# Performance work log

Measured on AMD Instinct MI355X. Metric: run time of the kernel, lower is better.

Reference implementation:

```python
import jax, jax.numpy as jnp
import numpy as np

INDIM, HID, OUTDIM, T = 28, 128, 10, 28

def setup_inputs() -> dict:
    key = jax.random.key(0)
    ks = jax.random.split(key, 7)
    B = 65536
    bound1 = 1.0 / np.sqrt(INDIM)
    bound2 = 1.0 / np.sqrt(2 * HID)
    bound3 = 1.0 / np.sqrt(HID)
    return {
        "x": jax.random.normal(ks[0], (B, 784), dtype=jnp.float32),
        "W1": jax.random.uniform(ks[1], (INDIM, HID), jnp.float32, -bound1, bound1),
        "b1": jax.random.uniform(ks[2], (HID,), jnp.float32, -bound1, bound1),
        "W2": jax.random.uniform(ks[3], (2 * HID, HID), jnp.float32, -bound2, bound2),
        "b2": jax.random.uniform(ks[4], (HID,), jnp.float32, -bound2, bound2),
        "W3": jax.random.uniform(ks[5], (HID, OUTDIM), jnp.float32, -bound3, bound3),
        "b3": jax.random.uniform(ks[6], (OUTDIM,), jnp.float32, -bound3, bound3),
    }

def reference(x, W1, b1, W2, b2, W3, b3):
    B = x.shape[0]
    # (B, 784) -> (T, B, 28): scan over the 28 rows of each image
    rows = jnp.transpose(x.reshape(B, T, INDIM), (1, 0, 2))
    # W2 split: first HID rows multiply linear1 output, last HID rows multiply hidden state
    W2a, W2b = W2[:HID], W2[HID:]

    def step(h, row):
        t = row @ W1 + b1                      # (B, HID)
        h_new = jax.nn.relu(t @ W2a + h @ W2b + b2)  # concat(t, h) @ W2 == t@W2a + h@W2b
        return h_new, None

    h0 = jnp.zeros((B, HID), dtype=x.dtype)
    h_final, _ = jax.lax.scan(step, h0, rows)
    return h_final @ W3 + b3
```

## Files before the change

kernel.cpp:

```cpp
#include <hip/hip_runtime.h>

#define BTOT 65536
#define TST  28
#define PACK_DW 180
#define WXL_OFF (64 * PACK_DW)

typedef __attribute__((ext_vector_type(8))) short bf16x8;
typedef __attribute__((ext_vector_type(4))) float f32x4;

__device__ __forceinline__ unsigned int f2bf(float f) {
    unsigned u = __float_as_uint(f);
    u += 0x7fff + ((u >> 16) & 1);
    return u >> 16;
}
__device__ __forceinline__ unsigned int pk2bf(float a, float b) {
    return f2bf(a) | (f2bf(b) << 16);
}
__device__ __forceinline__ bf16x8 cvt8(f32x4 a, f32x4 b) {
    union { unsigned int u[4]; bf16x8 v; } r;
    asm("v_cvt_pk_bf16_f32 %0, %1, %2" : "=v"(r.u[0]) : "v"(a[0]), "v"(a[1]));
    asm("v_cvt_pk_bf16_f32 %0, %1, %2" : "=v"(r.u[1]) : "v"(a[2]), "v"(a[3]));
    asm("v_cvt_pk_bf16_f32 %0, %1, %2" : "=v"(r.u[2]) : "v"(b[0]), "v"(b[1]));
    asm("v_cvt_pk_bf16_f32 %0, %1, %2" : "=v"(r.u[3]) : "v"(b[2]), "v"(b[3]));
    return r.v;
}


__global__ void pack1(const float* __restrict__ W1, const float* __restrict__ b1,
                      const float* __restrict__ W2, const float* __restrict__ b2,
                      const float* __restrict__ W3, const float* __restrict__ b3,
                      unsigned int* __restrict__ ws) {
    float* WxL = (float*)(ws + WXL_OFF);
    const int bid = blockIdx.x, tid = threadIdx.x;
    if (bid < 29) {
        const int k = bid, n = tid;
        float s = 0.f;
        if (k < 28) {
            for (int m = 0; m < 128; ++m) s += W1[k * 128 + m] * W2[m * 128 + n];
        } else {
            s = b2[n];
            for (int m = 0; m < 128; ++m) s += b1[m] * W2[m * 128 + n];
        }
        WxL[k * 128 + n] = s;
        if (k == 28) { WxL[29*128+n] = 0.f; WxL[30*128+n] = 0.f; WxL[31*128+n] = 0.f; }
    } else if (bid == 29) {
        if (tid < 64) {
            const int lr = tid & 15, kh = tid >> 4;
            unsigned int* P = ws + tid * PACK_DW;
            for (int kk = 0; kk < 4; ++kk)
                for (int t8 = 0; t8 < 8; ++t8)
                    for (int jd = 0; jd < 4; ++jd) {
                        const int s = kk * 32 + (jd >> 1) * 16 + kh * 4 + (jd & 1) * 2;
                        const int n = t8 * 16 + lr;
                        P[(kk * 8 + t8) * 4 + jd] =
                            pk2bf(W2[(128 + s) * 128 + n], W2[(129 + s) * 128 + n]);
                    }
        }
    } else {
        if (tid < 64) {
            const int lr = tid & 15, kh = tid >> 4;
            unsigned int* P = ws + tid * PACK_DW;
            for (int kk = 0; kk < 4; ++kk)
                for (int jd = 0; jd < 4; ++jd) {
                    const int s = kk * 32 + (jd >> 1) * 16 + kh * 4 + (jd & 1) * 2;
                    float lo = (lr < 10) ? W3[s * 10 + lr] : 0.f;
                    float hi = (lr < 10) ? W3[(s + 1) * 10 + lr] : 0.f;
                    P[160 + kk * 4 + jd] = pk2bf(lo, hi);
                }
            for (int j = 0; j < 4; ++j) {
                const int o = kh * 4 + j;
                P[176 + j] = __float_as_uint((o < 10) ? b3[o] : 0.f);
            }
        }
    }
}

__global__ void pack2(unsigned int* __restrict__ ws) {
    const int tid = threadIdx.x;
    if (tid < 64) {
        const float* WxL = (const float*)(ws + WXL_OFF);
        const int lr = tid & 15, kh = tid >> 4;
        unsigned int* P = ws + tid * PACK_DW;
        for (int t8 = 0; t8 < 8; ++t8)
            for (int jd = 0; jd < 4; ++jd) {
                const int k = kh * 8 + jd * 2, n = t8 * 16 + lr;
                P[128 + t8 * 4 + jd] = pk2bf(WxL[k * 128 + n], WxL[(k + 1) * 128 + n]);
            }
    }
}

__global__ __launch_bounds__(64, 2) void rnn_kernel(
    const float* __restrict__ x, const unsigned int* __restrict__ wsPack,
    float* __restrict__ out)
{
    const int lane = threadIdx.x;
    const int lr = lane & 15, kh = lane >> 4;
    const int r0 = blockIdx.x * 16;

    const unsigned int* P = wsPack + lane * PACK_DW;
    bf16x8 w2b[4][8], wx[8];
    #pragma unroll
    for (int kk = 0; kk < 4; ++kk)
        #pragma unroll
        for (int t8 = 0; t8 < 8; ++t8)
            w2b[kk][t8] = *(const bf16x8*)(P + (kk * 8 + t8) * 4);
    #pragma unroll
    for (int t8 = 0; t8 < 8; ++t8) wx[t8] = *(const bf16x8*)(P + 128 + t8 * 4);

    const f32x4 onec = {1.f, 0.f, 0.f, 0.f};
    const float* xr = x + (size_t)(r0 + lr) * 784 + 8 * kh;
    f32x4 xa = *(const f32x4*)xr;
    f32x4 xc = (kh < 3) ? *(const f32x4*)(xr + 4) : onec;
    bf16x8 xb = cvt8(xa, xc);
    const f32x4 z4 = {0.f, 0.f, 0.f, 0.f};

    f32x4 acc[8];
    union HF { unsigned int u[4]; bf16x8 v; } hb[4];
    f32x4 na, nc;

#define CVT(T8) do {                                                        \
        f32x4 v = acc[T8];                                                  \
        v[0] = fmaxf(v[0], 0.f); v[1] = fmaxf(v[1], 0.f);                   \
        v[2] = fmaxf(v[2], 0.f); v[3] = fmaxf(v[3], 0.f);                   \
        unsigned lo, hi;                                                    \
        asm("v_cvt_pk_bf16_f32 %0, %1, %2" : "=v"(lo) : "v"(v[0]), "v"(v[1])); \
        asm("v_cvt_pk_bf16_f32 %0, %1, %2" : "=v"(hi) : "v"(v[2]), "v"(v[3])); \
        hb[(T8) >> 1].u[((T8) & 1) * 2]     = lo;                           \
        hb[(T8) >> 1].u[((T8) & 1) * 2 + 1] = hi;                           \
    } while (0)
#define CVTALL  CVT(0); CVT(1); CVT(2); CVT(3); CVT(4); CVT(5); CVT(6); CVT(7)

    {
        const float* xp = xr + 28;
        na = *(const f32x4*)xp;
        nc = (kh < 3) ? *(const f32x4*)(xp + 4) : onec;
        __builtin_amdgcn_s_setprio(1);
        #pragma unroll
        for (int t8 = 0; t8 < 8; ++t8)
            acc[t8] = __builtin_amdgcn_mfma_f32_16x16x32_bf16(wx[t8], xb, z4, 0, 0, 0);
        __builtin_amdgcn_s_setprio(0);
        xb = cvt8(na, nc);
        CVTALL;
    }

    #pragma unroll 2
    for (int t = 1; t < TST; ++t) {
        const bool pf = (t + 1 < TST);
        if (pf) {
            const float* xp = xr + (t + 1) * 28;
            na = *(const f32x4*)xp;
            nc = (kh < 3) ? *(const f32x4*)(xp + 4) : onec;
        }
        __builtin_amdgcn_s_setprio(1);
        #pragma unroll
        for (int t8 = 0; t8 < 8; ++t8)
            acc[t8] = __builtin_amdgcn_mfma_f32_16x16x32_bf16(wx[t8], xb, z4, 0, 0, 0);
        #pragma unroll
        for (int kk = 0; kk < 4; ++kk)
            #pragma unroll
            for (int t8 = 0; t8 < 8; ++t8)
                acc[t8] = __builtin_amdgcn_mfma_f32_16x16x32_bf16(w2b[kk][t8], hb[kk].v, acc[t8], 0, 0, 0);
        __builtin_amdgcn_s_setprio(0);
        if (pf) xb = cvt8(na, nc);
        CVTALL;
    }

    bf16x8 w3f[4];
    #pragma unroll
    for (int kk = 0; kk < 4; ++kk) w3f[kk] = *(const bf16x8*)(P + 160 + kk * 4);
    const float* bp = (const float*)(P + 176);
    f32x4 accO = {bp[0], bp[1], bp[2], bp[3]};
    #pragma unroll
    for (int kk = 0; kk < 4; ++kk)
        accO = __builtin_amdgcn_mfma_f32_16x16x32_bf16(w3f[kk], hb[kk].v, accO, 0, 0, 0);
    float* op = out + (size_t)(r0 + lr) * 10 + kh * 4;
    #pragma unroll
    for (int j = 0; j < 4; ++j)
        if (kh * 4 + j < 10) op[j] = accO[j];

#undef CVT
#undef CVTALL
}

extern "C" void kernel_launch(void* const* d_in, const int* in_sizes, int n_in,
                              void* d_out, int out_size, void* d_ws, size_t ws_size,
                              hipStream_t stream) {
    const float* x  = (const float*)d_in[0];
    const float* W1 = (const float*)d_in[1];
    const float* b1 = (const float*)d_in[2];
    const float* W2 = (const float*)d_in[3];
    const float* b2 = (const float*)d_in[4];
    const float* W3 = (const float*)d_in[5];
    const float* b3 = (const float*)d_in[6];
    unsigned int* ws = (unsigned int*)d_ws;

    pack1<<<31, 128, 0, stream>>>(W1, b1, W2, b2, W3, b3, ws);
    pack2<<<1, 64, 0, stream>>>(ws);
    rnn_kernel<<<BTOT / 16, 64, 0, stream>>>(x, ws, (float*)d_out);
}
```

Measured before the change: 71.75 us.

## Interleave input-projection MFMAs for next step with relu/bf16 conversion of current step

Moves the x-projection MFMAs (wx times xb) for step t+1 out of the critical recurrent chain and issues them right after each pair of hidden-state conversions, so they overlap with the VALU relu/convert work. The loop is now fully unrolled. Each recurrent step then starts directly with the dependent W2b MFMAs. This aims to shorten the serial per-step latency, at the cost of larger code size and possibly more register pressure from full unrolling.

After: 76.27 us. 6.3% more time.

```diff
diff --git a/kernel.cpp b/kernel.cpp
--- a/kernel.cpp
+++ b/kernel.cpp
@@ -89,6 +89,8 @@
     }
 }
 
+#define MFMA(a, b, c) __builtin_amdgcn_mfma_f32_16x16x32_bf16(a, b, c, 0, 0, 0)
+
 __global__ __launch_bounds__(64, 2) void rnn_kernel(
     const float* __restrict__ x, const unsigned int* __restrict__ wsPack,
     float* __restrict__ out)
@@ -128,22 +130,27 @@
         hb[(T8) >> 1].u[((T8) & 1) * 2]     = lo;                           \
         hb[(T8) >> 1].u[((T8) & 1) * 2 + 1] = hi;                           \
     } while (0)
-#define CVTALL  CVT(0); CVT(1); CVT(2); CVT(3); CVT(4); CVT(5); CVT(6); CVT(7)
+#define CVT_REFILL(PAIR) do {                                               \
+        CVT(2 * (PAIR)); CVT(2 * (PAIR) + 1);                               \
+        acc[2 * (PAIR)]     = MFMA(wx[2 * (PAIR)],     xb, z4);             \
+        acc[2 * (PAIR) + 1] = MFMA(wx[2 * (PAIR) + 1], xb, z4);             \
+    } while (0)
 
     {
         const float* xp = xr + 28;
         na = *(const f32x4*)xp;
         nc = (kh < 3) ? *(const f32x4*)(xp + 4) : onec;
-        __builtin_amdgcn_s_setprio(1);
-        #pragma unroll
-        for (int t8 = 0; t8 < 8; ++t8)
-            acc[t8] = __builtin_amdgcn_mfma_f32_16x16x32_bf16(wx[t8], xb, z4, 0, 0, 0);
-        __builtin_amdgcn_s_setprio(0);
+        #pragma unroll
+        for (int t8 = 0; t8 < 8; ++t8)
+            acc[t8] = MFMA(wx[t8], xb, z4);
         xb = cvt8(na, nc);
-        CVTALL;
-    }
-
-    #pragma unroll 2
+        CVT(0); CVT(1); CVT(2); CVT(3); CVT(4); CVT(5); CVT(6); CVT(7);
+        #pragma unroll
+        for (int t8 = 0; t8 < 8; ++t8)
+            acc[t8] = MFMA(wx[t8], xb, z4);
+    }
+
+    #pragma unroll
     for (int t = 1; t < TST; ++t) {
         const bool pf = (t + 1 < TST);
         if (pf) {
@@ -153,16 +160,17 @@
         }
         __builtin_amdgcn_s_setprio(1);
         #pragma unroll
-        for (int t8 = 0; t8 < 8; ++t8)
-            acc[t8] = __builtin_amdgcn_mfma_f32_16x16x32_bf16(wx[t8], xb, z4, 0, 0, 0);
-        #pragma unroll
         for (int kk = 0; kk < 4; ++kk)
             #pragma unroll
             for (int t8 = 0; t8 < 8; ++t8)
-                acc[t8] = __builtin_amdgcn_mfma_f32_16x16x32_bf16(w2b[kk][t8], hb[kk].v, acc[t8], 0, 0, 0);
+                acc[t8] = MFMA(w2b[kk][t8], hb[kk].v, acc[t8]);
         __builtin_amdgcn_s_setprio(0);
-        if (pf) xb = cvt8(na, nc);
-        CVTALL;
+        if (pf) {
+            xb = cvt8(na, nc);
+            CVT_REFILL(0); CVT_REFILL(1); CVT_REFILL(2); CVT_REFILL(3);
+        } else {
+            CVT(0); CVT(1); CVT(2); CVT(3); CVT(4); CVT(5); CVT(6); CVT(7);
+        }
     }
 
     bf16x8 w3f[4];
@@ -172,14 +180,14 @@
     f32x4 accO = {bp[0], bp[1], bp[2], bp[3]};
     #pragma unroll
     for (int kk = 0; kk < 4; ++kk)
-        accO = __builtin_amdgcn_mfma_f32_16x16x32_bf16(w3f[kk], hb[kk].v, accO, 0, 0, 0);
+        accO = MFMA(w3f[kk], hb[kk].v, accO);
     float* op = out + (size_t)(r0 + lr) * 10 + kh * 4;
     #pragma unroll
     for (int j = 0; j < 4; ++j)
         if (kh * 4 + j < 10) op[j] = accO[j];
 
 #undef CVT
-#undef CVTALL
+#undef CVT_REFILL
 }
 
 extern "C" void kernel_launch(void* const* d_in, const int* in_sizes, int n_in,
```

## Switch recurrence to 32x32x16 MFMA tiles with 32 rows per wave

Applied to the files above, without the earlier changes.

Replaces the 16x16x32 bf16 MFMA formulation with 32x32x16 tiles, so each wave processes 32 batch rows instead of 16 and the grid halves. All weight packs are re-laid out for the new operand fragment layout, and the input-projection weights are staged in LDS rather than kept in registers, to make room for the larger accumulators. The aim is higher MFMA throughput per instruction and better reuse of the register-resident W2 fragments across more rows. The trade-offs are higher register pressure from the 16-wide accumulators, extra LDS reads every step, and fewer waves available to hide latency.

Result: slower. 85.64 us (+19.4%).

```diff
diff --git a/kernel.cpp b/kernel.cpp
--- a/kernel.cpp
+++ b/kernel.cpp
@@ -2,11 +2,13 @@
 
 #define BTOT 65536
 #define TST  28
-#define PACK_DW 180
+#define PACK_DW 208
 #define WXL_OFF (64 * PACK_DW)
 
-typedef __attribute__((ext_vector_type(8))) short bf16x8;
-typedef __attribute__((ext_vector_type(4))) float f32x4;
+typedef __attribute__((ext_vector_type(8)))  short bf16x8;
+typedef __attribute__((ext_vector_type(4)))  float f32x4;
+typedef __attribute__((ext_vector_type(16))) float f32x16;
+typedef __attribute__((ext_vector_type(4)))  unsigned int u32x4;
 
 __device__ __forceinline__ unsigned int f2bf(float f) {
     unsigned u = __float_as_uint(f);
@@ -45,31 +47,31 @@
         if (k == 28) { WxL[29*128+n] = 0.f; WxL[30*128+n] = 0.f; WxL[31*128+n] = 0.f; }
     } else if (bid == 29) {
         if (tid < 64) {
-            const int lr = tid & 15, kh = tid >> 4;
+            const int hi = tid >> 5, ln = tid & 31;
             unsigned int* P = ws + tid * PACK_DW;
-            for (int kk = 0; kk < 4; ++kk)
-                for (int t8 = 0; t8 < 8; ++t8)
+            for (int nt = 0; nt < 4; ++nt)
+                for (int ks = 0; ks < 8; ++ks)
                     for (int jd = 0; jd < 4; ++jd) {
-                        const int s = kk * 32 + (jd >> 1) * 16 + kh * 4 + (jd & 1) * 2;
-                        const int n = t8 * 16 + lr;
-                        P[(kk * 8 + t8) * 4 + jd] =
+                        const int s = 16 * ks + 8 * (jd >> 1) + 4 * hi + 2 * (jd & 1);
+                        const int n = 32 * nt + ln;
+                        P[(nt * 8 + ks) * 4 + jd] =
                             pk2bf(W2[(128 + s) * 128 + n], W2[(129 + s) * 128 + n]);
                     }
         }
     } else {
         if (tid < 64) {
-            const int lr = tid & 15, kh = tid >> 4;
+            const int hi = tid >> 5, ln = tid & 31;
             unsigned int* P = ws + tid * PACK_DW;
-            for (int kk = 0; kk < 4; ++kk)
+            for (int ks = 0; ks < 8; ++ks)
                 for (int jd = 0; jd < 4; ++jd) {
-                    const int s = kk * 32 + (jd >> 1) * 16 + kh * 4 + (jd & 1) * 2;
-                    float lo = (lr < 10) ? W3[s * 10 + lr] : 0.f;
-                    float hi = (lr < 10) ? W3[(s + 1) * 10 + lr] : 0.f;
-                    P[160 + kk * 4 + jd] = pk2bf(lo, hi);
+                    const int s = 16 * ks + 8 * (jd >> 1) + 4 * hi + 2 * (jd & 1);
+                    float lo = (ln < 10) ? W3[s * 10 + ln] : 0.f;
+                    float hh = (ln < 10) ? W3[(s + 1) * 10 + ln] : 0.f;
+                    P[160 + ks * 4 + jd] = pk2bf(lo, hh);
                 }
-            for (int j = 0; j < 4; ++j) {
-                const int o = kh * 4 + j;
-                P[176 + j] = __float_as_uint((o < 10) ? b3[o] : 0.f);
+            for (int r = 0; r < 16; ++r) {
+                const int row = (r & 3) + 8 * (r >> 2) + 4 * hi;
+                P[192 + r] = __float_as_uint((row < 10) ? b3[row] : 0.f);
             }
         }
     }
@@ -79,67 +81,83 @@
     const int tid = threadIdx.x;
     if (tid < 64) {
         const float* WxL = (const float*)(ws + WXL_OFF);
-        const int lr = tid & 15, kh = tid >> 4;
+        const int hi = tid >> 5, ln = tid & 31;
         unsigned int* P = ws + tid * PACK_DW;
-        for (int t8 = 0; t8 < 8; ++t8)
-            for (int jd = 0; jd < 4; ++jd) {
-                const int k = kh * 8 + jd * 2, n = t8 * 16 + lr;
-                P[128 + t8 * 4 + jd] = pk2bf(WxL[k * 128 + n], WxL[(k + 1) * 128 + n]);
-            }
-    }
-}
+        for (int nt = 0; nt < 4; ++nt)
+            for (int ks2 = 0; ks2 < 2; ++ks2)
+                for (int jd = 0; jd < 4; ++jd) {
+                    const int k = 16 * ks2 + 8 * hi + 2 * jd;
+                    const int n = 32 * nt + ln;
+                    P[128 + (nt * 2 + ks2) * 4 + jd] =
+                        pk2bf(WxL[k * 128 + n], WxL[(k + 1) * 128 + n]);
+                }
+    }
+}
+
+#define MFMA32(a, b, c) __builtin_amdgcn_mfma_f32_32x32x16_bf16(a, b, c, 0, 0, 0)
 
 __global__ __launch_bounds__(64, 2) void rnn_kernel(
     const float* __restrict__ x, const unsigned int* __restrict__ wsPack,
     float* __restrict__ out)
 {
+    __shared__ __align__(16) unsigned int wxLds[8 * 64 * 4];
     const int lane = threadIdx.x;
-    const int lr = lane & 15, kh = lane >> 4;
-    const int r0 = blockIdx.x * 16;
+    const int hi = lane >> 5, ln = lane & 31;
+    const int r0 = blockIdx.x * 32;
 
     const unsigned int* P = wsPack + lane * PACK_DW;
-    bf16x8 w2b[4][8], wx[8];
-    #pragma unroll
-    for (int kk = 0; kk < 4; ++kk)
-        #pragma unroll
-        for (int t8 = 0; t8 < 8; ++t8)
-            w2b[kk][t8] = *(const bf16x8*)(P + (kk * 8 + t8) * 4);
-    #pragma unroll
-    for (int t8 = 0; t8 < 8; ++t8) wx[t8] = *(const bf16x8*)(P + 128 + t8 * 4);
+    bf16x8 w2b[4][8];
+    #pragma unroll
+    for (int nt = 0; nt < 4; ++nt)
+        #pragma unroll
+        for (int ks = 0; ks < 8; ++ks)
+            w2b[nt][ks] = *(const bf16x8*)(P + (nt * 8 + ks) * 4);
+    #pragma unroll
+    for (int f = 0; f < 8; ++f) {
+        u32x4 v = *(const u32x4*)(P + 128 + f * 4);
+        *(u32x4*)&wxLds[(f * 64 + lane) * 4] = v;
+    }
 
     const f32x4 onec = {1.f, 0.f, 0.f, 0.f};
-    const float* xr = x + (size_t)(r0 + lr) * 784 + 8 * kh;
-    f32x4 xa = *(const f32x4*)xr;
-    f32x4 xc = (kh < 3) ? *(const f32x4*)(xr + 4) : onec;
-    bf16x8 xb = cvt8(xa, xc);
-    const f32x4 z4 = {0.f, 0.f, 0.f, 0.f};
-
-    f32x4 acc[8];
-    union HF { unsigned int u[4]; bf16x8 v; } hb[4];
-    f32x4 na, nc;
-
-#define CVT(T8) do {                                                        \
-        f32x4 v = acc[T8];                                                  \
-        v[0] = fmaxf(v[0], 0.f); v[1] = fmaxf(v[1], 0.f);                   \
-        v[2] = fmaxf(v[2], 0.f); v[3] = fmaxf(v[3], 0.f);                   \
-        unsigned lo, hi;                                                    \
-        asm("v_cvt_pk_bf16_f32 %0, %1, %2" : "=v"(lo) : "v"(v[0]), "v"(v[1])); \
-        asm("v_cvt_pk_bf16_f32 %0, %1, %2" : "=v"(hi) : "v"(v[2]), "v"(v[3])); \
-        hb[(T8) >> 1].u[((T8) & 1) * 2]     = lo;                           \
-        hb[(T8) >> 1].u[((T8) & 1) * 2 + 1] = hi;                           \
+    const float* xr = x + (size_t)(r0 + ln) * 784;
+    f32x4 q0 = *(const f32x4*)(xr + 8 * hi);
+    f32x4 q1 = *(const f32x4*)(xr + 8 * hi + 4);
+    f32x4 q2 = *(const f32x4*)(xr + 16 + 8 * hi);
+    f32x4 q3 = (hi == 0) ? *(const f32x4*)(xr + 20) : onec;
+    bf16x8 xb0 = cvt8(q0, q1);
+    bf16x8 xb1 = cvt8(q2, q3);
+    const f32x16 z16 = {0.f,0.f,0.f,0.f,0.f,0.f,0.f,0.f,0.f,0.f,0.f,0.f,0.f,0.f,0.f,0.f};
+
+    f32x16 acc[4];
+    union HF { unsigned int u[4]; bf16x8 v; } hbF[8];
+    f32x4 n0, n1, n2, n3;
+
+#define CVT1(NT, P8) do {                                                   \
+        float a0 = fmaxf(acc[NT][2 * (P8)],     0.f);                       \
+        float a1 = fmaxf(acc[NT][2 * (P8) + 1], 0.f);                       \
+        unsigned d;                                                         \
+        asm("v_cvt_pk_bf16_f32 %0, %1, %2" : "=v"(d) : "v"(a0), "v"(a1));   \
+        hbF[2 * (NT) + ((P8) >> 2)].u[(P8) & 3] = d;                        \
     } while (0)
-#define CVTALL  CVT(0); CVT(1); CVT(2); CVT(3); CVT(4); CVT(5); CVT(6); CVT(7)
+#define CVTTILE(NT) CVT1(NT,0); CVT1(NT,1); CVT1(NT,2); CVT1(NT,3); \
+                    CVT1(NT,4); CVT1(NT,5); CVT1(NT,6); CVT1(NT,7)
+#define CVTALL CVTTILE(0); CVTTILE(1); CVTTILE(2); CVTTILE(3)
 
     {
         const float* xp = xr + 28;
-        na = *(const f32x4*)xp;
-        nc = (kh < 3) ? *(const f32x4*)(xp + 4) : onec;
-        __builtin_amdgcn_s_setprio(1);
-        #pragma unroll
-        for (int t8 = 0; t8 < 8; ++t8)
-            acc[t8] = __builtin_amdgcn_mfma_f32_16x16x32_bf16(wx[t8], xb, z4, 0, 0, 0);
-        __builtin_amdgcn_s_setprio(0);
-        xb = cvt8(na, nc);
+        n0 = *(const f32x4*)(xp + 8 * hi);
+        n1 = *(const f32x4*)(xp + 8 * hi + 4);
+        n2 = *(const f32x4*)(xp + 16 + 8 * hi);
+        n3 = (hi == 0) ? *(const f32x4*)(xp + 20) : onec;
+        #pragma unroll
+        for (int nt = 0; nt < 4; ++nt) {
+            bf16x8 wa = *(const bf16x8*)&wxLds[((nt * 2) * 64 + lane) * 4];
+            bf16x8 wb = *(const bf16x8*)&wxLds[((nt * 2 + 1) * 64 + lane) * 4];
+            acc[nt] = MFMA32(wa, xb0, z16);
+            acc[nt] = MFMA32(wb, xb1, acc[nt]);
+        }
+        xb0 = cvt8(n0, n1);
+        xb1 = cvt8(n2, n3);
         CVTALL;
     }
 
@@ -148,37 +166,51 @@
         const bool pf = (t + 1 < TST);
         if (pf) {
             const float* xp = xr + (t + 1) * 28;
-            na = *(const f32x4*)xp;
-            nc = (kh < 3) ? *(const f32x4*)(xp + 4) : onec;
+            n0 = *(const f32x4*)(xp + 8 * hi);
+            n1 = *(const f32x4*)(xp + 8 * hi + 4);
+            n2 = *(const f32x4*)(xp + 16 + 8 * hi);
+            n3 = (hi == 0) ? *(const f32x4*)(xp + 20) : onec;
         }
         __builtin_amdgcn_s_setprio(1);
         #pragma unroll
-        for (int t8 = 0; t8 < 8; ++t8)
-            acc[t8] = __builtin_amdgcn_mfma_f32_16x16x32_bf16(wx[t8], xb, z4, 0, 0, 0);
-        #pragma unroll
-        for (int kk = 0; kk < 4; ++kk)
+        for (int nt = 0; nt < 4; ++nt) {
+            bf16x8 wa = *(const bf16x8*)&wxLds[((nt * 2) * 64 + lane) * 4];
+            bf16x8 wb = *(const bf16x8*)&wxLds[((nt * 2 + 1) * 64 + lane) * 4];
+            acc[nt] = MFMA32(wa, xb0, z16);
+            acc[nt] = MFMA32(wb, xb1, acc[nt]);
+        }
+        #pragma unroll
+        for (int ks = 0; ks < 8; ++ks)
             #pragma unroll
-            for (int t8 = 0; t8 < 8; ++t8)
-                acc[t8] = __builtin_amdgcn_mfma_f32_16x16x32_bf16(w2b[kk][t8], hb[kk].v, acc[t8], 0, 0, 0);
+            for (int nt = 0; nt < 4; ++nt)
+                acc[nt] = MFMA32(w2b[nt][ks], hbF[ks].v, acc[nt]);
         __builtin_amdgcn_s_setprio(0);
-        if (pf) xb = cvt8(na, nc);
+        if (pf) {
+            xb0 = cvt8(n0, n1);
+            xb1 = cvt8(n2, n3);
+        }
         CVTALL;
     }
 
-    bf16x8 w3f[4];
-    #pragma unroll
-    for (int kk = 0; kk < 4; ++kk) w3f[kk] = *(const bf16x8*)(P + 160 + kk * 4);
-    const float* bp = (const float*)(P + 176);
-    f32x4 accO = {bp[0], bp[1], bp[2], bp[3]};
-    #pragma unroll
-    for (int kk = 0; kk < 4; ++kk)
-        accO = __builtin_amdgcn_mfma_f32_16x16x32_bf16(w3f[kk], hb[kk].v, accO, 0, 0, 0);
-    float* op = out + (size_t)(r0 + lr) * 10 + kh * 4;
-    #pragma unroll
-    for (int j = 0; j < 4; ++j)
-        if (kh * 4 + j < 10) op[j] = accO[j];
-
-#undef CVT
+    bf16x8 w3f[8];
+    #pragma unroll
+    for (int ks = 0; ks < 8; ++ks) w3f[ks] = *(const bf16x8*)(P + 160 + ks * 4);
+    const float* bp = (const float*)(P + 192);
+    f32x16 accO;
+    #pragma unroll
+    for (int r = 0; r < 16; ++r) accO[r] = bp[r];
+    #pragma unroll
+    for (int ks = 0; ks < 8; ++ks)
+        accO = MFMA32(w3f[ks], hbF[ks].v, accO);
+    float* op = out + (size_t)(r0 + ln) * 10;
+    #pragma unroll
+    for (int r = 0; r < 16; ++r) {
+        const int row = (r & 3) + 8 * (r >> 2) + 4 * hi;
+        if (row < 10) op[row] = accO[r];
+    }
+
+#undef CVT1
+#undef CVTTILE
 #undef CVTALL
 }
 
@@ -196,5 +228,5 @@
 
     pack1<<<31, 128, 0, stream>>>(W1, b1, W2, b2, W3, b3, ws);
     pack2<<<1, 64, 0, stream>>>(ws);
-    rnn_kernel<<<BTOT / 16, 64, 0, stream>>>(x, ws, (float*)d_out);
-}
+    rnn_kernel<<<BTOT / 32, 64, 0, stream>>>(x, ws, (float*)d_out);
+}
```
